# Optimization experiments

Measured on AMD Instinct MI355X. Metric: run time of the kernel, lower is better.

The kernel has to match this reference:

```python
import jax, jax.numpy as jnp
import numpy as np

# Fixed 6-node graph from the module (source -> target, PyG convention)
SRC = jnp.array([1, 2, 0, 2, 1, 3, 2, 4, 3, 5, 3, 4], dtype=jnp.int32)
DST = jnp.array([0, 0, 1, 1, 2, 2, 3, 3, 4, 4, 5, 5], dtype=jnp.int32)
N_NODES = 6
FEAT = 64
BATCH = 131072


def _gcn_norm(fill_value):
    # add self loops with weight fill_value (improved=True -> 2.0)
    src = jnp.concatenate([SRC, jnp.arange(N_NODES, dtype=jnp.int32)])
    dst = jnp.concatenate([DST, jnp.arange(N_NODES, dtype=jnp.int32)])
    w = jnp.concatenate([jnp.ones(12, jnp.float32), jnp.full((N_NODES,), fill_value, jnp.float32)])
    deg = jnp.zeros((N_NODES,), jnp.float32).at[dst].add(w)
    dinv = jnp.where(deg > 0, jax.lax.rsqrt(deg), 0.0)
    norm = dinv[src] * w * dinv[dst]  # [18]
    return src, dst, norm


def _gcn_conv(x, W, b, fill_value):
    # x: [B, N, F]; PyG GCNConv: h = x @ W^T, aggregate norm * h[src] at dst, add bias
    h = jnp.einsum('bnf,gf->bng', x, W)
    src, dst, norm = _gcn_norm(fill_value)
    msg = h[:, src, :] * norm[None, :, None]          # [B, 18, F]
    out = jnp.zeros_like(h).at[:, dst, :].add(msg)     # scatter-add over targets
    return out + b


def setup_inputs() -> dict:
    key = jax.random.key(0)
    ks = jax.random.split(key, 12)
    s = 1.0 / np.sqrt(FEAT)
    inp = {'x': jax.random.normal(ks[0], (BATCH, N_NODES, FEAT), jnp.float32)}
    for i in range(4):
        inp[f'W{i+1}'] = jax.random.uniform(ks[1 + 2 * i], (FEAT, FEAT), jnp.float32, -s, s)
        inp[f'b{i+1}'] = jax.random.uniform(ks[2 + 2 * i], (FEAT,), jnp.float32, -s, s)
    inp['fc_w'] = jax.random.uniform(ks[9], (N_NODES, FEAT), jnp.float32, -s, s)  # 6 stacked Linear(64,1) weights
    inp['fc_b'] = jax.random.uniform(ks[10], (N_NODES,), jnp.float32, -s, s)
    return inp


def reference(x, W1, b1, W2, b2, W3, b3, W4, b4, fc_w, fc_b):
    h = jax.nn.relu(_gcn_conv(x, W1, b1, 1.0))
    h = jax.nn.relu(_gcn_conv(h, W2, b2, 1.0))
    h = jax.nn.relu(_gcn_conv(h, W3, b3, 2.0))  # improved=True
    h = jax.nn.relu(_gcn_conv(h, W4, b4, 2.0))  # improved=True
    r = h + x  # residual
    # per-node Linear(64,1) heads, concatenated -> [B, 6]
    logits = jnp.einsum('bnf,nf->bn', r, fc_w) + fc_b
    return jax.nn.sigmoid(logits)
```

## Files before the change

### kernel.cpp

```cpp
#include <hip/hip_runtime.h>

typedef __attribute__((ext_vector_type(8))) _Float16 f16x8;
typedef __attribute__((ext_vector_type(2))) __fp16 fp16x2;
typedef __attribute__((ext_vector_type(4))) float f32x4;

union U8 { f16x8 v; fp16x2 p[4]; };

__device__ __forceinline__ f16x8 cvt8(f32x4 a, f32x4 b) {
  U8 u;
  u.p[0] = __builtin_amdgcn_cvt_pkrtz(a.x, a.y);
  u.p[1] = __builtin_amdgcn_cvt_pkrtz(a.z, a.w);
  u.p[2] = __builtin_amdgcn_cvt_pkrtz(b.x, b.y);
  u.p[3] = __builtin_amdgcn_cvt_pkrtz(b.z, b.w);
  return u.v;
}

__device__ __forceinline__ float dot4(f32x4 a, f32x4 b) {
  return a.x * b.x + a.y * b.y + a.z * b.z + a.w * b.w;
}

#define PAD 80

__global__ __launch_bounds__(256, 8) void gcn_fused(
    const float* __restrict__ x,
    const float* __restrict__ W1, const float* __restrict__ B1,
    const float* __restrict__ W2, const float* __restrict__ B2,
    const float* __restrict__ W3, const float* __restrict__ B3,
    const float* __restrict__ W4, const float* __restrict__ B4,
    const float* __restrict__ fcw, const float* __restrict__ fcb,
    float* __restrict__ out)
{
  __shared__ __align__(16) _Float16 xs[6][16][PAD];
  __shared__ float pacc_s[6][16];
  __shared__ float ls[16][6];

  const int tid  = threadIdx.x;
  const int lane = tid & 63;
  const int w    = tid >> 6;
  const int c    = lane & 15;
  const int q    = lane >> 4;
  const int b0   = blockIdx.x * 16;

  const int CONS[6][4] = {{0,1,-1,-1},{0,1,2,-1},{0,1,2,3},{2,3,4,5},{3,4,5,-1},{4,5,-1,-1}};
  const float* Ws[4] = {W1, W2, W3, W4};
  const float* Bs[4] = {B1, B2, B3, B4};

  {
    const float* xb = x + (size_t)b0 * 384;
#pragma unroll
    for (int r = 0; r < 3; ++r) {
      const int i = tid * 8 + r * 2048;
      const int b = i / 384;
      const int rem = i - b * 384;
      const int n = rem >> 6;
      const int f = rem & 63;
      f32x4 v0 = *(const f32x4*)(xb + i);
      f32x4 v1 = *(const f32x4*)(xb + i + 4);
      const float* fw = fcw + n * 64 + f;
      float p = dot4(v0, *(const f32x4*)fw) + dot4(v1, *(const f32x4*)(fw + 4));
      p += __shfl_xor(p, 1, 64);
      p += __shfl_xor(p, 2, 64);
      p += __shfl_xor(p, 4, 64);
      if ((tid & 7) == 0) pacc_s[n][b] = p;
      *(f16x8*)&xs[n][b][f] = cvt8(v0, v1);
    }
  }
  __syncthreads();

  f32x4 acc[6];

#pragma unroll
  for (int l = 0; l < 4; ++l) {
    const float cbv = (l < 2) ? (1.f / 3.f) : 0.25f;
    const float* wp = Ws[l] + (w * 16 + c) * 64 + q * 8;
    f32x4 u0 = *(const f32x4*)wp        * cbv;
    f32x4 u1 = *(const f32x4*)(wp + 4)  * cbv;
    f32x4 u2 = *(const f32x4*)(wp + 32) * cbv;
    f32x4 u3 = *(const f32x4*)(wp + 36) * cbv;
    f16x8 wb0 = cvt8(u0, u1), wb1 = cvt8(u2, u3);
    f16x8 wa0, wa1;
    if (l < 2) { wa0 = wb0; wa1 = wb1; }
    else       { wa0 = wb0 + wb0; wa1 = wb1 + wb1; }
    const float bv = Bs[l][w * 16 + c];
    const f32x4 bc = {bv, bv, bv, bv};
#pragma unroll
    for (int n = 0; n < 6; ++n) acc[n] = bc;

#pragma unroll
    for (int m = 0; m < 6; ++m) {
      f16x8 a0 = *(const f16x8*)&xs[m][c][q * 8];
      f16x8 a1 = *(const f16x8*)&xs[m][c][q * 8 + 32];
#pragma unroll
      for (int j = 0; j < 4; ++j) {
        const int n = CONS[m][j];
        if (n >= 0) {
          acc[n] = __builtin_amdgcn_mfma_f32_16x16x32_f16(a0, (n == m) ? wa0 : wb0, acc[n], 0, 0, 0);
          acc[n] = __builtin_amdgcn_mfma_f32_16x16x32_f16(a1, (n == m) ? wa1 : wb1, acc[n], 0, 0, 0);
        }
      }
    }
    __syncthreads();
#pragma unroll
    for (int n = 0; n < 6; ++n)
#pragma unroll
      for (int e = 0; e < 4; ++e)
        xs[n][q * 4 + e][w * 16 + c] = (_Float16)fmaxf(acc[n][e], 0.f);
    __syncthreads();
  }

  const f32x4 z4 = {0.f, 0.f, 0.f, 0.f};
  for (int n = w; n < 6; n += 4) {
    f16x8 a0 = *(const f16x8*)&xs[n][c][q * 8];
    f16x8 a1 = *(const f16x8*)&xs[n][c][q * 8 + 32];
    const float* fw = fcw + n * 64 + q * 8;
    f16x8 bf0 = cvt8(*(const f32x4*)fw,        *(const f32x4*)(fw + 4));
    f16x8 bf1 = cvt8(*(const f32x4*)(fw + 32), *(const f32x4*)(fw + 36));
    f32x4 sv = __builtin_amdgcn_mfma_f32_16x16x32_f16(a0, bf0, z4, 0, 0, 0);
    sv = __builtin_amdgcn_mfma_f32_16x16x32_f16(a1, bf1, sv, 0, 0, 0);
    if (c == 0) {
      const float fb = fcb[n];
#pragma unroll
      for (int e = 0; e < 4; ++e) {
        const float v = sv[e] + pacc_s[n][q * 4 + e] + fb;
        ls[q * 4 + e][n] = 1.f / (1.f + __expf(-v));
      }
    }
  }
  __syncthreads();
  if (tid < 96) out[(size_t)b0 * 6 + tid] = ((const float*)ls)[tid];
}

extern "C" void kernel_launch(void* const* d_in, const int* in_sizes, int n_in,
                              void* d_out, int out_size, void* d_ws, size_t ws_size,
                              hipStream_t stream) {
  const float* x   = (const float*)d_in[0];
  const float* W1  = (const float*)d_in[1];
  const float* B1  = (const float*)d_in[2];
  const float* W2  = (const float*)d_in[3];
  const float* B2  = (const float*)d_in[4];
  const float* W3  = (const float*)d_in[5];
  const float* B3  = (const float*)d_in[6];
  const float* W4  = (const float*)d_in[7];
  const float* B4  = (const float*)d_in[8];
  const float* fcw = (const float*)d_in[9];
  const float* fcb = (const float*)d_in[10];
  float* out = (float*)d_out;

  const int batch  = in_sizes[0] / (6 * 64);
  const int blocks = batch / 16;
  hipLaunchKernelGGL(gcn_fused, dim3(blocks), dim3(256), 0, stream,
                     x, W1, B1, W2, B2, W3, B3, W4, B4, fcw, fcb, out);
}
```

Before: 88.06 us.

## Double batch tile per block, swizzle LDS layout, and swap MFMA operands

Each block now processes 32 batch rows instead of 16. Each wave reuses its converted weight fragments across two 16-row MFMA tiles, which halves the per-row cost of weight loads and conversions. The padded LDS layout is replaced by an XOR-swizzled 64-wide layout to avoid bank conflicts. MFMA operands are swapped so the relu writeback can store packed f16x4 vectors instead of scalar halves. In exchange it uses more registers (two accumulator sets) and lowers the occupancy hint from 8 to 4 blocks per CU.

```diff
diff --git a/kernel.cpp b/kernel.cpp
--- a/kernel.cpp
+++ b/kernel.cpp
@@ -1,10 +1,12 @@
 #include <hip/hip_runtime.h>
 
 typedef __attribute__((ext_vector_type(8))) _Float16 f16x8;
+typedef __attribute__((ext_vector_type(4))) _Float16 f16x4;
 typedef __attribute__((ext_vector_type(2))) __fp16 fp16x2;
 typedef __attribute__((ext_vector_type(4))) float f32x4;
 
 union U8 { f16x8 v; fp16x2 p[4]; };
+union U4 { f16x4 v; fp16x2 p[2]; };
 
 __device__ __forceinline__ f16x8 cvt8(f32x4 a, f32x4 b) {
   U8 u;
@@ -14,14 +16,19 @@
   u.p[3] = __builtin_amdgcn_cvt_pkrtz(b.z, b.w);
   return u.v;
 }
-
+__device__ __forceinline__ f16x4 cvt4(f32x4 a) {
+  U4 u;
+  u.p[0] = __builtin_amdgcn_cvt_pkrtz(a.x, a.y);
+  u.p[1] = __builtin_amdgcn_cvt_pkrtz(a.z, a.w);
+  return u.v;
+}
 __device__ __forceinline__ float dot4(f32x4 a, f32x4 b) {
   return a.x * b.x + a.y * b.y + a.z * b.z + a.w * b.w;
 }
 
-#define PAD 80
+#define BT 32
 
-__global__ __launch_bounds__(256, 8) void gcn_fused(
+__global__ __launch_bounds__(256, 4) void gcn_fused(
     const float* __restrict__ x,
     const float* __restrict__ W1, const float* __restrict__ B1,
     const float* __restrict__ W2, const float* __restrict__ B2,
@@ -30,16 +37,16 @@
     const float* __restrict__ fcw, const float* __restrict__ fcb,
     float* __restrict__ out)
 {
-  __shared__ __align__(16) _Float16 xs[6][16][PAD];
-  __shared__ float pacc_s[6][16];
-  __shared__ float ls[16][6];
+  __shared__ __align__(16) _Float16 xs[6 * BT * 64];
+  __shared__ float pacc_s[6][BT];
+  __shared__ float ls[BT][6];
 
   const int tid  = threadIdx.x;
   const int lane = tid & 63;
   const int w    = tid >> 6;
   const int c    = lane & 15;
   const int q    = lane >> 4;
-  const int b0   = blockIdx.x * 16;
+  const int b0   = blockIdx.x * BT;
 
   const int CONS[6][4] = {{0,1,-1,-1},{0,1,2,-1},{0,1,2,3},{2,3,4,5},{3,4,5,-1},{4,5,-1,-1}};
   const float* Ws[4] = {W1, W2, W3, W4};
@@ -48,7 +55,7 @@
   {
     const float* xb = x + (size_t)b0 * 384;
 #pragma unroll
-    for (int r = 0; r < 3; ++r) {
+    for (int r = 0; r < 6; ++r) {
       const int i = tid * 8 + r * 2048;
       const int b = i / 384;
       const int rem = i - b * 384;
@@ -62,12 +69,16 @@
       p += __shfl_xor(p, 2, 64);
       p += __shfl_xor(p, 4, 64);
       if ((tid & 7) == 0) pacc_s[n][b] = p;
-      *(f16x8*)&xs[n][b][f] = cvt8(v0, v1);
+      const int slot = (f >> 3) ^ (b & 7);
+      *(f16x8*)&xs[(n * BT + b) * 64 + slot * 8] = cvt8(v0, v1);
     }
   }
   __syncthreads();
 
-  f32x4 acc[6];
+  f32x4 acc[2][6];
+  const int s1 = (q ^ (c & 7)) * 8;
+  const int s2 = ((q + 4) ^ (c & 7)) * 8;
+  const int wsl = ((w * 2 + (q >> 1)) ^ (c & 7)) * 8 + (q & 1) * 4;
 
 #pragma unroll
   for (int l = 0; l < 4; ++l) {
@@ -81,53 +92,64 @@
     f16x8 wa0, wa1;
     if (l < 2) { wa0 = wb0; wa1 = wb1; }
     else       { wa0 = wb0 + wb0; wa1 = wb1 + wb1; }
-    const float bv = Bs[l][w * 16 + c];
-    const f32x4 bc = {bv, bv, bv, bv};
+    const f32x4 bval = *(const f32x4*)(Bs[l] + w * 16 + q * 4);
 #pragma unroll
-    for (int n = 0; n < 6; ++n) acc[n] = bc;
+    for (int hh = 0; hh < 2; ++hh)
+#pragma unroll
+      for (int n = 0; n < 6; ++n) acc[hh][n] = bval;
 
 #pragma unroll
     for (int m = 0; m < 6; ++m) {
-      f16x8 a0 = *(const f16x8*)&xs[m][c][q * 8];
-      f16x8 a1 = *(const f16x8*)&xs[m][c][q * 8 + 32];
 #pragma unroll
-      for (int j = 0; j < 4; ++j) {
-        const int n = CONS[m][j];
-        if (n >= 0) {
-          acc[n] = __builtin_amdgcn_mfma_f32_16x16x32_f16(a0, (n == m) ? wa0 : wb0, acc[n], 0, 0, 0);
-          acc[n] = __builtin_amdgcn_mfma_f32_16x16x32_f16(a1, (n == m) ? wa1 : wb1, acc[n], 0, 0, 0);
+      for (int hh = 0; hh < 2; ++hh) {
+        const int row = (m * BT + hh * 16 + c) * 64;
+        f16x8 a0 = *(const f16x8*)&xs[row + s1];
+        f16x8 a1 = *(const f16x8*)&xs[row + s2];
+#pragma unroll
+        for (int j = 0; j < 4; ++j) {
+          const int n = CONS[m][j];
+          if (n >= 0) {
+            acc[hh][n] = __builtin_amdgcn_mfma_f32_16x16x32_f16((n == m) ? wa0 : wb0, a0, acc[hh][n], 0, 0, 0);
+            acc[hh][n] = __builtin_amdgcn_mfma_f32_16x16x32_f16((n == m) ? wa1 : wb1, a1, acc[hh][n], 0, 0, 0);
+          }
         }
       }
     }
     __syncthreads();
 #pragma unroll
-    for (int n = 0; n < 6; ++n)
+    for (int hh = 0; hh < 2; ++hh) {
+      const int brow = hh * 16 + c;
 #pragma unroll
-      for (int e = 0; e < 4; ++e)
-        xs[n][q * 4 + e][w * 16 + c] = (_Float16)fmaxf(acc[n][e], 0.f);
+      for (int n = 0; n < 6; ++n) {
+        f32x4 r;
+#pragma unroll
+        for (int e = 0; e < 4; ++e) r[e] = fmaxf(acc[hh][n][e], 0.f);
+        *(f16x4*)&xs[(n * BT + brow) * 64 + wsl] = cvt4(r);
+      }
+    }
     __syncthreads();
   }
 
   const f32x4 z4 = {0.f, 0.f, 0.f, 0.f};
-  for (int n = w; n < 6; n += 4) {
-    f16x8 a0 = *(const f16x8*)&xs[n][c][q * 8];
-    f16x8 a1 = *(const f16x8*)&xs[n][c][q * 8 + 32];
+#pragma unroll
+  for (int u = w; u < 12; u += 4) {
+    const int n = u % 6;
+    const int hh = u / 6;
+    const int row = (n * BT + hh * 16 + c) * 64;
+    f16x8 hb0 = *(const f16x8*)&xs[row + s1];
+    f16x8 hb1 = *(const f16x8*)&xs[row + s2];
     const float* fw = fcw + n * 64 + q * 8;
-    f16x8 bf0 = cvt8(*(const f32x4*)fw,        *(const f32x4*)(fw + 4));
-    f16x8 bf1 = cvt8(*(const f32x4*)(fw + 32), *(const f32x4*)(fw + 36));
-    f32x4 sv = __builtin_amdgcn_mfma_f32_16x16x32_f16(a0, bf0, z4, 0, 0, 0);
-    sv = __builtin_amdgcn_mfma_f32_16x16x32_f16(a1, bf1, sv, 0, 0, 0);
-    if (c == 0) {
-      const float fb = fcb[n];
-#pragma unroll
-      for (int e = 0; e < 4; ++e) {
-        const float v = sv[e] + pacc_s[n][q * 4 + e] + fb;
-        ls[q * 4 + e][n] = 1.f / (1.f + __expf(-v));
-      }
+    f16x8 fa0 = cvt8(*(const f32x4*)fw,        *(const f32x4*)(fw + 4));
+    f16x8 fa1 = cvt8(*(const f32x4*)(fw + 32), *(const f32x4*)(fw + 36));
+    f32x4 sv = __builtin_amdgcn_mfma_f32_16x16x32_f16(fa0, hb0, z4, 0, 0, 0);
+    sv = __builtin_amdgcn_mfma_f32_16x16x32_f16(fa1, hb1, sv, 0, 0, 0);
+    if (q == 0) {
+      const float v = sv[0] + pacc_s[n][hh * 16 + c] + fcb[n];
+      ls[hh * 16 + c][n] = 1.f / (1.f + __expf(-v));
     }
   }
   __syncthreads();
-  if (tid < 96) out[(size_t)b0 * 6 + tid] = ((const float*)ls)[tid];
+  if (tid < 192) out[(size_t)b0 * 6 + tid] = ((const float*)ls)[tid];
 }
 
 extern "C" void kernel_launch(void* const* d_in, const int* in_sizes, int n_in,
@@ -147,7 +169,7 @@
   float* out = (float*)d_out;
 
   const int batch  = in_sizes[0] / (6 * 64);
-  const int blocks = batch / 16;
+  const int blocks = batch / BT;
   hipLaunchKernelGGL(gcn_fused, dim3(blocks), dim3(256), 0, stream,
                      x, W1, B1, W2, B2, W3, B3, W4, B4, fcw, fcb, out);
 }
```

New measurement: 77.59 us. -11.9%, faster.
